# Performance work log

Measured on AMD Instinct MI355X. Metric: run time of the kernel, lower is better.

The kernel has to match this reference:

```python
import jax, jax.numpy as jnp
import numpy as np

D_MODEL = 2048
NUM_HEADS = 16
D_K = D_MODEL // NUM_HEADS
THETA = 10000.0
BATCH, SEQ = 2, 2048


def setup_inputs() -> dict:
    key = jax.random.key(0)
    ks = jax.random.split(key, 5)
    scale = 1.0 / np.sqrt(D_MODEL)
    x = jax.random.normal(ks[0], (BATCH, SEQ, D_MODEL), dtype=jnp.float32)
    token_positions = jnp.broadcast_to(jnp.arange(SEQ, dtype=jnp.int32)[None, :], (BATCH, SEQ))
    Wq = jax.random.normal(ks[1], (D_MODEL, D_MODEL), dtype=jnp.float32) * scale
    Wk = jax.random.normal(ks[2], (D_MODEL, D_MODEL), dtype=jnp.float32) * scale
    Wv = jax.random.normal(ks[3], (D_MODEL, D_MODEL), dtype=jnp.float32) * scale
    Wo = jax.random.normal(ks[4], (D_MODEL, D_MODEL), dtype=jnp.float32) * scale
    return {"x": x, "token_positions": token_positions, "Wq": Wq, "Wk": Wk, "Wv": Wv, "Wo": Wo}


def _apply_rope(t, positions):
    # t: [b, h, s, d_k]; positions: [b, s]. Interleaved-pair rotation.
    half = D_K // 2
    inv_freq = THETA ** (-jnp.arange(0, half, dtype=jnp.float32) * 2.0 / D_K)  # [half]
    ang = positions.astype(jnp.float32)[:, :, None] * inv_freq[None, None, :]  # [b, s, half]
    cos = jnp.cos(ang)[:, None, :, :]  # [b, 1, s, half]
    sin = jnp.sin(ang)[:, None, :, :]
    t2 = t.reshape(*t.shape[:-1], half, 2)
    x1, x2 = t2[..., 0], t2[..., 1]
    r1 = x1 * cos - x2 * sin
    r2 = x1 * sin + x2 * cos
    return jnp.stack([r1, r2], axis=-1).reshape(t.shape)


def reference(x, token_positions, Wq, Wk, Wv, Wo):
    b, s, _ = x.shape
    # Linear layers compute x @ W^T (weight stored as [out, in], no bias)
    def proj(w):
        y = jnp.einsum('bsd,ed->bse', x, w)
        return y.reshape(b, s, NUM_HEADS, D_K).transpose(0, 2, 1, 3)  # b h s d
    Q, K, V = proj(Wq), proj(Wk), proj(Wv)
    Q = _apply_rope(Q, token_positions)
    K = _apply_rope(K, token_positions)
    scores = jnp.einsum('bhqd,bhkd->bhqk', Q, K) / jnp.sqrt(jnp.float32(D_K))
    causal = jnp.tril(jnp.ones((s, s), dtype=bool))
    scores = jnp.where(causal[None, None], scores, jnp.finfo(scores.dtype).min)
    attn = jax.nn.softmax(scores, axis=-1)
    out = jnp.einsum('bhqk,bhkd->bhqd', attn, V)  # b h s d
    out = out.transpose(0, 2, 1, 3).reshape(b, s, D_MODEL)
    return jnp.einsum('bse,de->bsd', out, Wo)
```

## Files before the change

kernel.cpp:

```cpp
#include <hip/hip_runtime.h>
#include <cstdint>
#include <cstddef>

#define D_MODEL 2048
#define NHEAD 16
#define DK 128
#define SEQ 2048
#define BATCH 2
#define NTOK (BATCH * SEQ)
#define NQB 32

typedef __bf16 bf16;
typedef __bf16 bf16x2 __attribute__((ext_vector_type(2)));
typedef __bf16 bf16x4 __attribute__((ext_vector_type(4)));
typedef __bf16 bf16x8 __attribute__((ext_vector_type(8)));
typedef float f32x4 __attribute__((ext_vector_type(4)));

__device__ __forceinline__ void g2lds16(const void* g, void* l) {
  __builtin_amdgcn_global_load_lds(
      (const __attribute__((address_space(1))) void*)g,
      (__attribute__((address_space(3))) void*)l, 16, 0, 0);
}

__device__ __forceinline__ void cstore(float* p, float v) { *p = v; }
__device__ __forceinline__ void cstore(bf16* p, float v) { *p = (bf16)v; }

#define BAR()                              \
  {                                        \
    asm volatile("" ::: "memory");         \
    __builtin_amdgcn_s_barrier();          \
    asm volatile("" ::: "memory");         \
  }

__global__ void k_conv5(const float* __restrict__ X, const float* __restrict__ W0,
                        const float* __restrict__ W1, const float* __restrict__ W2,
                        const float* __restrict__ W3, bf16* __restrict__ xo,
                        bf16* __restrict__ o0, bf16* __restrict__ o1,
                        bf16* __restrict__ o2, bf16* __restrict__ o3,
                        int nx4, int nw4) {
  const float* in;
  bf16* out;
  int n;
  switch (blockIdx.y) {
    case 0: in = X; out = xo; n = nx4; break;
    case 1: in = W0; out = o0; n = nw4; break;
    case 2: in = W1; out = o1; n = nw4; break;
    case 3: in = W2; out = o2; n = nw4; break;
    default: in = W3; out = o3; n = nw4;
  }
  int i = blockIdx.x * blockDim.x + threadIdx.x;
  if (i >= n) return;
  const float4 v = ((const float4*)in)[i];
  bf16x4 o = {(bf16)v.x, (bf16)v.y, (bf16)v.z, (bf16)v.w};
  ((bf16x4*)out)[i] = o;
}

__global__ __launch_bounds__(512, 1) void k_gemm8(
    const bf16* __restrict__ A, const bf16* __restrict__ B0p, const bf16* __restrict__ B1p,
    const bf16* __restrict__ B2p, bf16* __restrict__ C0, bf16* __restrict__ C1,
    bf16* __restrict__ C2, const int* __restrict__ pos, int M, int N, int K) {
  const bf16* Bp = B0p;
  bf16* Cp = C0;
  if (blockIdx.z == 1) { Bp = B1p; Cp = C1; }
  else if (blockIdx.z == 2) { Bp = B2p; Cp = C2; }
  const bool rope = (blockIdx.z < 2);

  __shared__ bf16 Ab[2][256 * 64];
  __shared__ bf16 Bb[2][256 * 64];

  const int t = threadIdx.x;
  const int wid = t >> 6, lane = t & 63;
  const int wr = wid >> 2, wc = wid & 3;
  const int lr = lane & 15, lg = lane >> 4;
  const int bm = blockIdx.y, bn = blockIdx.x;
  const size_t arow0 = (size_t)bm * 256;
  const size_t brow0 = (size_t)bn * 256;

  const int srow = wid * 8 + (lane >> 3);
  const int schunk = ((lane & 7) ^ ((lane >> 3) & 7)) * 8;

#define STG(X, row0, k0, lb, h)                                                \
  {                                                                            \
    g2lds16(&(X)[((row0) + (h)*128 + srow) * (size_t)K + (k0) + schunk],       \
            &(lb)[((h)*128 + wid * 8) * 64]);                                  \
    g2lds16(&(X)[((row0) + (h)*128 + 64 + srow) * (size_t)K + (k0) + schunk],  \
            &(lb)[((h)*128 + 64 + wid * 8) * 64]);                             \
  }
#define LDA8(lb, mh, m, kk) \
  (*(const bf16x8*)&(lb)[((mh)*128 + wr * 64 + (m)*16 + lr) * 64 + ((((kk)*4 + lg) ^ (lr & 7)) * 8)])
#define LDB8(lb, nh, n, kk) \
  (*(const bf16x8*)&(lb)[((nh)*128 + wc * 32 + (n)*16 + lr) * 64 + ((((kk)*4 + lg) ^ (lr & 7)) * 8)])

  const int T = K >> 6;

  STG(A, arow0, 0, Ab[0], 0);
  STG(A, arow0, 0, Ab[0], 1);
  STG(Bp, brow0, 0, Bb[0], 0);
  STG(Bp, brow0, 0, Bb[0], 1);
  STG(A, arow0, 64, Ab[1], 0);

  f32x4 acc[2][2][4][2] = {};

  for (int tt = 0; tt < T; ++tt) {
    const int cur = tt & 1;
    const bf16* Ac = Ab[cur];
    const bf16* Bc = Bb[cur];
    bf16* Aw = Ab[cur];
    bf16* An = Ab[cur ^ 1];
    bf16* Bn = Bb[cur ^ 1];
    const int k1 = (tt + 1) << 6;
    const int k2 = (tt + 2) << 6;
    const bool pf1 = (tt + 1 < T);
    const bool pf2 = (tt + 2 < T);

    if (tt == T - 1) {
      asm volatile("s_waitcnt vmcnt(0)" ::: "memory");
    } else {
      asm volatile("s_waitcnt vmcnt(2)" ::: "memory");
    }
    BAR();

    bf16x8 a[4][2], b0[2][2], b1[2][2];

#pragma unroll
    for (int m = 0; m < 4; ++m)
#pragma unroll
      for (int kk = 0; kk < 2; ++kk) a[m][kk] = LDA8(Ac, 0, m, kk);
#pragma unroll
    for (int n = 0; n < 2; ++n)
#pragma unroll
      for (int kk = 0; kk < 2; ++kk) b0[n][kk] = LDB8(Bc, 0, n, kk);
    if (pf1) {
      STG(A, arow0, k1, An, 1);
      STG(Bp, brow0, k1, Bn, 0);
    }
    __builtin_amdgcn_s_setprio(1);
#pragma unroll
    for (int m = 0; m < 4; ++m)
#pragma unroll
      for (int n = 0; n < 2; ++n)
#pragma unroll
        for (int kk = 0; kk < 2; ++kk)
          acc[0][0][m][n] =
              __builtin_amdgcn_mfma_f32_16x16x32_bf16(a[m][kk], b0[n][kk], acc[0][0][m][n], 0, 0, 0);
    __builtin_amdgcn_s_setprio(0);
    BAR();

#pragma unroll
    for (int n = 0; n < 2; ++n)
#pragma unroll
      for (int kk = 0; kk < 2; ++kk) b1[n][kk] = LDB8(Bc, 1, n, kk);
    if (pf1) STG(Bp, brow0, k1, Bn, 1);
    __builtin_amdgcn_s_setprio(1);
#pragma unroll
    for (int m = 0; m < 4; ++m)
#pragma unroll
      for (int n = 0; n < 2; ++n)
#pragma unroll
        for (int kk = 0; kk < 2; ++kk)
          acc[0][1][m][n] =
              __builtin_amdgcn_mfma_f32_16x16x32_bf16(a[m][kk], b1[n][kk], acc[0][1][m][n], 0, 0, 0);
    __builtin_amdgcn_s_setprio(0);
    BAR();

#pragma unroll
    for (int m = 0; m < 4; ++m)
#pragma unroll
      for (int kk = 0; kk < 2; ++kk) a[m][kk] = LDA8(Ac, 1, m, kk);
    if (pf2) STG(A, arow0, k2, Aw, 0);
    __builtin_amdgcn_s_setprio(1);
#pragma unroll
    for (int m = 0; m < 4; ++m)
#pragma unroll
      for (int n = 0; n < 2; ++n)
#pragma unroll
        for (int kk = 0; kk < 2; ++kk)
          acc[1][1][m][n] =
              __builtin_amdgcn_mfma_f32_16x16x32_bf16(a[m][kk], b1[n][kk], acc[1][1][m][n], 0, 0, 0);
    __builtin_amdgcn_s_setprio(0);
    BAR();

    __builtin_amdgcn_s_setprio(1);
#pragma unroll
    for (int m = 0; m < 4; ++m)
#pragma unroll
      for (int n = 0; n < 2; ++n)
#pragma unroll
        for (int kk = 0; kk < 2; ++kk)
          acc[1][0][m][n] =
              __builtin_amdgcn_mfma_f32_16x16x32_bf16(a[m][kk], b0[n][kk], acc[1][0][m][n], 0, 0, 0);
    __builtin_amdgcn_s_setprio(0);
  }

  float invf[2];
#pragma unroll
  for (int n = 0; n < 2; ++n) {
    int f = ((wc * 32 + n * 16 + lr) & 127) >> 1;
    invf[n] = exp2f((float)f * -0.20762050593121503f);
  }
#pragma unroll
  for (int mh = 0; mh < 2; ++mh)
#pragma unroll
    for (int m = 0; m < 4; ++m) {
      size_t rowb = arow0 + mh * 128 + wr * 64 + m * 16 + lg * 4;
#pragma unroll
      for (int r = 0; r < 4; ++r) {
        float p = rope ? (float)pos[rowb + r] : 0.0f;
#pragma unroll
        for (int n = 0; n < 2; ++n) {
          float sn, cs;
          if (rope) __sincosf(p * invf[n], &sn, &cs);
#pragma unroll
          for (int nh = 0; nh < 2; ++nh) {
            float v = acc[mh][nh][m][n][r];
            float vp = __shfl_xor(v, 1);
            float outv = v;
            if (rope) outv = (lr & 1) ? (v * cs + vp * sn) : (v * cs - vp * sn);
            size_t col = brow0 + nh * 128 + wc * 32 + n * 16 + lr;
            Cp[(rowb + r) * N + col] = (bf16)outv;
          }
        }
      }
    }
#undef STG
#undef LDA8
#undef LDB8
}

template <typename OutT>
__global__ __launch_bounds__(256, 2) void k_gemm_nt(
    const bf16* __restrict__ A, const bf16* __restrict__ B0, const bf16* __restrict__ B1,
    const bf16* __restrict__ B2, OutT* __restrict__ C0, OutT* __restrict__ C1,
    OutT* __restrict__ C2, int M, int N, int K) {
  const bf16* Bp = B0;
  OutT* Cp = C0;
  if (blockIdx.z == 1) { Bp = B1; Cp = C1; }
  else if (blockIdx.z == 2) { Bp = B2; Cp = C2; }

  __shared__ bf16 As[128 * 32];
  __shared__ bf16 Bs[128 * 32];

  const int t = threadIdx.x;
  const int w = t >> 6;
  const int lane = t & 63;
  const int lr = lane & 15;
  const int lg = lane >> 4;
  const int wr = w >> 1, wc = w & 1;
  const int bm = blockIdx.y, bn = blockIdx.x;

  f32x4 acc[4][4] = {};

  const int srow = lane >> 2;
  const int scol = (lane & 3) * 8;

  const int kt_iters = K >> 5;
  for (int kt = 0; kt < kt_iters; ++kt) {
    const int kbase = kt * 32;
#pragma unroll
    for (int i = 0; i < 2; ++i) {
      int chunk = w * 2 + i;
      int row = chunk * 16 + srow;
      g2lds16(&A[(size_t)(bm * 128 + row) * K + kbase + scol], &As[chunk * 512]);
      g2lds16(&Bp[(size_t)(bn * 128 + row) * K + kbase + scol], &Bs[chunk * 512]);
    }
    asm volatile("s_waitcnt vmcnt(0)" ::: "memory");
    __syncthreads();

    bf16x8 af[4], bfr[4];
#pragma unroll
    for (int m = 0; m < 4; ++m)
      af[m] = *(const bf16x8*)&As[(wr * 64 + m * 16 + lr) * 32 + lg * 8];
#pragma unroll
    for (int n = 0; n < 4; ++n)
      bfr[n] = *(const bf16x8*)&Bs[(wc * 64 + n * 16 + lr) * 32 + lg * 8];
#pragma unroll
    for (int m = 0; m < 4; ++m)
#pragma unroll
      for (int n = 0; n < 4; ++n)
        acc[m][n] = __builtin_amdgcn_mfma_f32_16x16x32_bf16(af[m], bfr[n], acc[m][n], 0, 0, 0);
    __syncthreads();
  }

#pragma unroll
  for (int m = 0; m < 4; ++m) {
    int rowb = bm * 128 + wr * 64 + m * 16 + lg * 4;
#pragma unroll
    for (int n = 0; n < 4; ++n) {
      int col = bn * 128 + wc * 64 + n * 16 + lr;
#pragma unroll
      for (int r = 0; r < 4; ++r) cstore(&Cp[(size_t)(rowb + r) * N + col], acc[m][n][r]);
    }
  }
}

__global__ __launch_bounds__(256, 2) void k_attn(const bf16* __restrict__ Q,
                                                 const bf16* __restrict__ K,
                                                 const bf16* __restrict__ V,
                                                 bf16* __restrict__ O) {
  const int wg = blockIdx.x;
  const int g = wg & 7;
  const int i = wg >> 3;
  const int bh = g + 8 * (i & 3);
  const int pr = i >> 2;
  const int b = bh >> 4, h = bh & 15;

  const int t = threadIdx.x;
  const int w = t >> 6, lane = t & 63;
  const int lr = lane & 15, lg = lane >> 4;

  const size_t rowbase = (size_t)b * SEQ;
  const int hoff = h * DK;

  __shared__ bf16 Ks[2][64 * 128];
  __shared__ uint32_t VTu[2][128 * 32];
  __shared__ bf16 Pb[4][16 * 64];

  const int kp = t & 31;
  const int d0s = (t >> 5) * 16;

  const float scale = 0.08838834764831845f;
  const float FIXM = 8.0f;

  bf16x8 sa0, sa1, sb0, sb1;
  int cur = 0;

  const int krow_l = lane >> 4;
  const int kchunk = lane & 15;

  for (int qsel = 0; qsel < 2; ++qsel) {
    const int qblk = qsel ? pr : (NQB - 1 - pr);
    const int qb = qblk * 64;
    const int ktiles = qblk + 1;

    bf16x8 qf[4];
    {
      size_t qrow = rowbase + qb + w * 16 + lr;
#pragma unroll
      for (int c = 0; c < 4; ++c)
        qf[c] = *(const bf16x8*)&Q[qrow * D_MODEL + hoff + c * 32 + lg * 8];
    }

    f32x4 o[8] = {};
    f32x4 lrow = {};

#pragma unroll
    for (int j = 0; j < 4; ++j) {
      int row = w * 16 + j * 4 + krow_l;
      int chunk = kchunk ^ (j * 4 + krow_l);
      g2lds16(&K[(rowbase + row) * D_MODEL + hoff + chunk * 8],
              &Ks[cur][(size_t)(w * 16 + j * 4) * 128]);
    }
    {
      const bf16* vp0 = &V[(rowbase + 2 * kp) * D_MODEL + hoff + d0s];
      sa0 = *(const bf16x8*)vp0;
      sa1 = *(const bf16x8*)(vp0 + 8);
      sb0 = *(const bf16x8*)(vp0 + D_MODEL);
      sb1 = *(const bf16x8*)(vp0 + D_MODEL + 8);
    }

    for (int kt = 0; kt < ktiles; ++kt) {
      const int k0 = kt * 64;
#pragma unroll
      for (int j = 0; j < 8; ++j) {
        int d = d0s + j;
        bf16x2 p0 = {sa0[j], sb0[j]};
        VTu[cur][d * 32 + (kp ^ ((d & 7) << 2))] = *(const uint32_t*)&p0;
      }
#pragma unroll
      for (int j = 0; j < 8; ++j) {
        int d = d0s + 8 + j;
        bf16x2 p1 = {sa1[j], sb1[j]};
        VTu[cur][d * 32 + (kp ^ ((d & 7) << 2))] = *(const uint32_t*)&p1;
      }
      asm volatile("s_waitcnt vmcnt(0)" ::: "memory");
      __syncthreads();

      if (kt + 1 < ktiles) {
#pragma unroll
        for (int j = 0; j < 4; ++j) {
          int row = w * 16 + j * 4 + krow_l;
          int chunk = kchunk ^ (j * 4 + krow_l);
          g2lds16(&K[(rowbase + k0 + 64 + row) * D_MODEL + hoff + chunk * 8],
                  &Ks[cur ^ 1][(size_t)(w * 16 + j * 4) * 128]);
        }
        const bf16* vp0 = &V[(rowbase + k0 + 64 + 2 * kp) * D_MODEL + hoff + d0s];
        sa0 = *(const bf16x8*)vp0;
        sa1 = *(const bf16x8*)(vp0 + 8);
        sb0 = *(const bf16x8*)(vp0 + D_MODEL);
        sb1 = *(const bf16x8*)(vp0 + D_MODEL + 8);
      }

      f32x4 sc[4];
      __builtin_amdgcn_s_setprio(1);
#pragma unroll
      for (int tt = 0; tt < 4; ++tt) {
        f32x4 a = {};
#pragma unroll
        for (int c = 0; c < 4; ++c) {
          bf16x8 kf = *(const bf16x8*)&Ks[cur][(tt * 16 + lr) * 128 + (((c * 4 + lg) ^ lr) * 8)];
          a = __builtin_amdgcn_mfma_f32_16x16x32_bf16(qf[c], kf, a, 0, 0, 0);
        }
        sc[tt] = a * scale;
      }
      __builtin_amdgcn_s_setprio(0);

      const int qrow0 = qb + w * 16 + lg * 4;
      if (k0 + 64 > qb + w * 16) {
#pragma unroll
        for (int tt = 0; tt < 4; ++tt) {
          int kcol = k0 + tt * 16 + lr;
#pragma unroll
          for (int r = 0; r < 4; ++r)
            if (kcol > qrow0 + r) sc[tt][r] = -3.0e38f;
        }
      }

#pragma unroll
      for (int tt = 0; tt < 4; ++tt)
#pragma unroll
        for (int r = 0; r < 4; ++r) {
          float p = __expf(sc[tt][r] - FIXM);
          sc[tt][r] = p;
          lrow[r] += p;
        }

#pragma unroll
      for (int tt = 0; tt < 4; ++tt)
#pragma unroll
        for (int r = 0; r < 4; ++r) {
          int q = lg * 4 + r;
          int col = tt * 16 + lr;
          Pb[w][q * 64 + (col ^ ((q & 7) << 3))] = (bf16)sc[tt][r];
        }
      asm volatile("s_waitcnt lgkmcnt(0)" ::: "memory");
      bf16x8 pf0 = *(const bf16x8*)&Pb[w][lr * 64 + ((lg * 8) ^ ((lr & 7) << 3))];
      bf16x8 pf1 = *(const bf16x8*)&Pb[w][lr * 64 + ((32 + lg * 8) ^ ((lr & 7) << 3))];

      __builtin_amdgcn_s_setprio(1);
#pragma unroll
      for (int nt = 0; nt < 8; ++nt) {
        int d = nt * 16 + lr;
        bf16x8 vf0 = *(const bf16x8*)&VTu[cur][d * 32 + ((lg * 4) ^ ((d & 7) << 2))];
        bf16x8 vf1 = *(const bf16x8*)&VTu[cur][d * 32 + ((16 + lg * 4) ^ ((d & 7) << 2))];
        o[nt] = __builtin_amdgcn_mfma_f32_16x16x32_bf16(pf0, vf0, o[nt], 0, 0, 0);
        o[nt] = __builtin_amdgcn_mfma_f32_16x16x32_bf16(pf1, vf1, o[nt], 0, 0, 0);
      }
      __builtin_amdgcn_s_setprio(0);
      cur ^= 1;
    }

#pragma unroll
    for (int off = 8; off >= 1; off >>= 1)
#pragma unroll
      for (int r = 0; r < 4; ++r) lrow[r] += __shfl_xor(lrow[r], off);

    size_t orow = rowbase + qb + w * 16 + lg * 4;
#pragma unroll
    for (int nt = 0; nt < 8; ++nt)
#pragma unroll
      for (int r = 0; r < 4; ++r)
        O[(orow + r) * D_MODEL + hoff + nt * 16 + lr] = (bf16)(o[nt][r] / lrow[r]);
  }
}

extern "C" void kernel_launch(void* const* d_in, const int* in_sizes, int n_in, void* d_out,
                              int out_size, void* d_ws, size_t ws_size, hipStream_t stream) {
  const float* x = (const float*)d_in[0];
  const int* pos = (const int*)d_in[1];
  const float* Wq = (const float*)d_in[2];
  const float* Wk = (const float*)d_in[3];
  const float* Wv = (const float*)d_in[4];
  const float* Wo = (const float*)d_in[5];
  float* out = (float*)d_out;

  char* ws = (char*)d_ws;
  const size_t MB = 1u << 20;
  bf16* xb  = (bf16*)(ws);
  bf16* wqb = (bf16*)(ws + 16 * MB);
  bf16* wkb = (bf16*)(ws + 24 * MB);
  bf16* wvb = (bf16*)(ws + 32 * MB);
  bf16* wob = (bf16*)(ws + 40 * MB);
  bf16* Qb  = (bf16*)(ws + 48 * MB);
  bf16* Kb  = (bf16*)(ws + 64 * MB);
  bf16* Vb  = (bf16*)(ws + 80 * MB);
  bf16* AOb = (bf16*)(ws + 96 * MB);

  {
    int nx4 = NTOK * D_MODEL / 4;
    int nw4 = D_MODEL * D_MODEL / 4;
    k_conv5<<<dim3((nx4 + 255) / 256, 5), 256, 0, stream>>>(
        x, Wq, Wk, Wv, Wo, xb, wqb, wkb, wvb, wob, nx4, nw4);
  }
  {
    dim3 g(D_MODEL / 256, NTOK / 256, 3);
    k_gemm8<<<g, 512, 0, stream>>>(xb, wqb, wkb, wvb, Qb, Kb, Vb, pos,
                                   NTOK, D_MODEL, D_MODEL);
  }
  k_attn<<<dim3(NQB * NHEAD * BATCH / 2, 1, 1), 256, 0, stream>>>(Qb, Kb, Vb, AOb);
  {
    dim3 g(D_MODEL / 128, NTOK / 128, 1);
    k_gemm_nt<float><<<g, 256, 0, stream>>>(AOb, wob, wob, wob, out, out, out, NTOK, D_MODEL, D_MODEL);
  }
}
```

Before: 265.0 us.

## Split V projection into separate 128x256-tile GEMM and drop mid-loop barriers

Moves the V projection out of the fused QKV GEMM into a new kernel that uses 128x256 output tiles, so 256 workgroups (one per CU) run instead of a third slice of the big-tile launch. It also removes two barriers and a priority toggle inside the k_gemm8 main loop to cut synchronisation stalls. Removing the barriers risks LDS races between prefetch writes and fragment reads, and the extra launch adds overhead.

```diff
diff --git a/kernel.cpp b/kernel.cpp
--- a/kernel.cpp
+++ b/kernel.cpp
@@ -161,7 +161,6 @@
           acc[0][1][m][n] =
               __builtin_amdgcn_mfma_f32_16x16x32_bf16(a[m][kk], b1[n][kk], acc[0][1][m][n], 0, 0, 0);
     __builtin_amdgcn_s_setprio(0);
-    BAR();
 
 #pragma unroll
     for (int m = 0; m < 4; ++m)
@@ -177,10 +176,7 @@
         for (int kk = 0; kk < 2; ++kk)
           acc[1][1][m][n] =
               __builtin_amdgcn_mfma_f32_16x16x32_bf16(a[m][kk], b1[n][kk], acc[1][1][m][n], 0, 0, 0);
-    __builtin_amdgcn_s_setprio(0);
-    BAR();
-
-    __builtin_amdgcn_s_setprio(1);
+
 #pragma unroll
     for (int m = 0; m < 4; ++m)
 #pragma unroll
@@ -223,6 +219,165 @@
       }
     }
 #undef STG
+#undef LDA8
+#undef LDB8
+}
+
+__global__ __launch_bounds__(512, 1) void k_gemmPV(
+    const bf16* __restrict__ A, const bf16* __restrict__ Bp, bf16* __restrict__ Cp,
+    int M, int N, int K) {
+  const int wg = blockIdx.x;
+  const int bn = wg & 7;
+  const int bm = wg >> 3;
+
+  __shared__ bf16 Ab[2][128 * 64];
+  __shared__ bf16 Bb[2][256 * 64];
+
+  const int t = threadIdx.x;
+  const int wid = t >> 6, lane = t & 63;
+  const int wr = wid >> 2, wc = wid & 3;
+  const int lr = lane & 15, lg = lane >> 4;
+  const size_t arow0 = (size_t)bm * 128;
+  const size_t brow0 = (size_t)bn * 256;
+
+  const int srow = wid * 8 + (lane >> 3);
+  const int schunk = ((lane & 7) ^ ((lane >> 3) & 7)) * 8;
+
+#define STGA(X, k0, lb, h) \
+  g2lds16(&(X)[(arow0 + (h)*64 + srow) * (size_t)K + (k0) + schunk], &(lb)[((h)*64 + wid * 8) * 64]);
+#define STGB(X, k0, lb, h)                                                        \
+  {                                                                               \
+    g2lds16(&(X)[(brow0 + (h)*128 + srow) * (size_t)K + (k0) + schunk],           \
+            &(lb)[((h)*128 + wid * 8) * 64]);                                     \
+    g2lds16(&(X)[(brow0 + (h)*128 + 64 + srow) * (size_t)K + (k0) + schunk],      \
+            &(lb)[((h)*128 + 64 + wid * 8) * 64]);                                \
+  }
+#define LDA8(lb, mh, m, kk) \
+  (*(const bf16x8*)&(lb)[((mh)*64 + wr * 32 + (m)*16 + lr) * 64 + ((((kk)*4 + lg) ^ (lr & 7)) * 8)])
+#define LDB8(lb, nh, n, kk) \
+  (*(const bf16x8*)&(lb)[((nh)*128 + wc * 32 + (n)*16 + lr) * 64 + ((((kk)*4 + lg) ^ (lr & 7)) * 8)])
+
+  const int T = K >> 6;
+
+  STGA(A, 0, Ab[0], 0);
+  STGA(A, 0, Ab[0], 1);
+  STGB(Bp, 0, Bb[0], 0);
+  STGB(Bp, 0, Bb[0], 1);
+  STGA(A, 64, Ab[1], 0);
+
+  f32x4 acc[2][2][2][2] = {};
+
+  for (int tt = 0; tt < T; ++tt) {
+    const int cur = tt & 1;
+    const bf16* Ac = Ab[cur];
+    const bf16* Bc = Bb[cur];
+    bf16* Aw = Ab[cur];
+    bf16* An = Ab[cur ^ 1];
+    bf16* Bn = Bb[cur ^ 1];
+    const int k1 = (tt + 1) << 6;
+    const int k2 = (tt + 2) << 6;
+    const bool pf1 = (tt + 1 < T);
+    const bool pf2 = (tt + 2 < T);
+
+    if (tt == T - 1) {
+      asm volatile("s_waitcnt vmcnt(0)" ::: "memory");
+    } else {
+      asm volatile("s_waitcnt vmcnt(1)" ::: "memory");
+    }
+    BAR();
+
+    bf16x8 a[2][2], b[2][2];
+
+#pragma unroll
+    for (int m = 0; m < 2; ++m)
+#pragma unroll
+      for (int kk = 0; kk < 2; ++kk) a[m][kk] = LDA8(Ac, 0, m, kk);
+#pragma unroll
+    for (int n = 0; n < 2; ++n)
+#pragma unroll
+      for (int kk = 0; kk < 2; ++kk) b[n][kk] = LDB8(Bc, 0, n, kk);
+    if (pf1) {
+      STGA(A, k1, An, 1);
+      STGB(Bp, k1, Bn, 0);
+    }
+    __builtin_amdgcn_s_setprio(1);
+#pragma unroll
+    for (int m = 0; m < 2; ++m)
+#pragma unroll
+      for (int n = 0; n < 2; ++n)
+#pragma unroll
+        for (int kk = 0; kk < 2; ++kk)
+          acc[0][0][m][n] =
+              __builtin_amdgcn_mfma_f32_16x16x32_bf16(a[m][kk], b[n][kk], acc[0][0][m][n], 0, 0, 0);
+    __builtin_amdgcn_s_setprio(0);
+    BAR();
+
+#pragma unroll
+    for (int n = 0; n < 2; ++n)
+#pragma unroll
+      for (int kk = 0; kk < 2; ++kk) b[n][kk] = LDB8(Bc, 1, n, kk);
+    if (pf1) STGB(Bp, k1, Bn, 1);
+    __builtin_amdgcn_s_setprio(1);
+#pragma unroll
+    for (int m = 0; m < 2; ++m)
+#pragma unroll
+      for (int n = 0; n < 2; ++n)
+#pragma unroll
+        for (int kk = 0; kk < 2; ++kk)
+          acc[0][1][m][n] =
+              __builtin_amdgcn_mfma_f32_16x16x32_bf16(a[m][kk], b[n][kk], acc[0][1][m][n], 0, 0, 0);
+    __builtin_amdgcn_s_setprio(0);
+    BAR();
+
+#pragma unroll
+    for (int m = 0; m < 2; ++m)
+#pragma unroll
+      for (int kk = 0; kk < 2; ++kk) a[m][kk] = LDA8(Ac, 1, m, kk);
+    if (pf2) STGA(A, k2, Aw, 0);
+    __builtin_amdgcn_s_setprio(1);
+#pragma unroll
+    for (int m = 0; m < 2; ++m)
+#pragma unroll
+      for (int n = 0; n < 2; ++n)
+#pragma unroll
+        for (int kk = 0; kk < 2; ++kk)
+          acc[1][1][m][n] =
+              __builtin_amdgcn_mfma_f32_16x16x32_bf16(a[m][kk], b[n][kk], acc[1][1][m][n], 0, 0, 0);
+    __builtin_amdgcn_s_setprio(0);
+    BAR();
+
+#pragma unroll
+    for (int n = 0; n < 2; ++n)
+#pragma unroll
+      for (int kk = 0; kk < 2; ++kk) b[n][kk] = LDB8(Bc, 0, n, kk);
+    __builtin_amdgcn_s_setprio(1);
+#pragma unroll
+    for (int m = 0; m < 2; ++m)
+#pragma unroll
+      for (int n = 0; n < 2; ++n)
+#pragma unroll
+        for (int kk = 0; kk < 2; ++kk)
+          acc[1][0][m][n] =
+              __builtin_amdgcn_mfma_f32_16x16x32_bf16(a[m][kk], b[n][kk], acc[1][0][m][n], 0, 0, 0);
+    __builtin_amdgcn_s_setprio(0);
+  }
+
+#pragma unroll
+  for (int mh = 0; mh < 2; ++mh)
+#pragma unroll
+    for (int nh = 0; nh < 2; ++nh)
+#pragma unroll
+      for (int m = 0; m < 2; ++m) {
+        size_t rowb = arow0 + mh * 64 + wr * 32 + m * 16 + lg * 4;
+#pragma unroll
+        for (int n = 0; n < 2; ++n) {
+          size_t col = brow0 + nh * 128 + wc * 32 + n * 16 + lr;
+#pragma unroll
+          for (int r = 0; r < 4; ++r) Cp[(rowb + r) * N + col] = (bf16)acc[mh][nh][m][n][r];
+        }
+      }
+#undef STGA
+#undef STGB
 #undef LDA8
 #undef LDB8
 }
@@ -492,10 +647,11 @@
         x, Wq, Wk, Wv, Wo, xb, wqb, wkb, wvb, wob, nx4, nw4);
   }
   {
-    dim3 g(D_MODEL / 256, NTOK / 256, 3);
-    k_gemm8<<<g, 512, 0, stream>>>(xb, wqb, wkb, wvb, Qb, Kb, Vb, pos,
+    dim3 g(D_MODEL / 256, NTOK / 256, 2);
+    k_gemm8<<<g, 512, 0, stream>>>(xb, wqb, wkb, wkb, Qb, Kb, Kb, pos,
                                    NTOK, D_MODEL, D_MODEL);
   }
+  k_gemmPV<<<256, 512, 0, stream>>>(xb, wvb, Vb, NTOK, D_MODEL, D_MODEL);
   k_attn<<<dim3(NQB * NHEAD * BATCH / 2, 1, 1), 256, 0, stream>>>(Qb, Kb, Vb, AOb);
   {
     dim3 g(D_MODEL / 128, NTOK / 128, 1);
```

After: 261.7 us. No clear change (-1.2%).
